# Kernel optimization log

Hardware: AMD Instinct MI355X
Metric: run time of the kernel (lower is better)

The kernel has to match this reference:

```python
import jax, jax.numpy as jnp
import numpy as np

N = 50000
E = 800000
IN_DIM = 128
HID = 128
HEADS = 8
OUT_DIM = 64
LRELU_SLOPE = 0.2


def setup_inputs() -> dict:
    key = jax.random.key(0)
    ks = jax.random.split(key, 10)
    x = jax.random.normal(ks[0], (N, IN_DIM), dtype=jnp.float32)
    edge_index = jax.random.randint(ks[1], (2, E), 0, N, dtype=jnp.int64)
    c1 = HID // HEADS  # 16
    W1 = jax.random.normal(ks[2], (IN_DIM, HID), dtype=jnp.float32) * (1.0 / np.sqrt(IN_DIM))
    as1 = jax.random.normal(ks[3], (HEADS, c1), dtype=jnp.float32) * 0.1
    ad1 = jax.random.normal(ks[4], (HEADS, c1), dtype=jnp.float32) * 0.1
    b1 = jnp.zeros((HID,), dtype=jnp.float32)
    W2 = jax.random.normal(ks[5], (HID, OUT_DIM), dtype=jnp.float32) * (1.0 / np.sqrt(HID))
    as2 = jax.random.normal(ks[6], (1, OUT_DIM), dtype=jnp.float32) * 0.1
    ad2 = jax.random.normal(ks[7], (1, OUT_DIM), dtype=jnp.float32) * 0.1
    b2 = jnp.zeros((OUT_DIM,), dtype=jnp.float32)
    return {"x": x, "edge_index": edge_index, "W1": W1, "as1": as1, "ad1": ad1,
            "b1": b1, "W2": W2, "as2": as2, "ad2": ad2, "b2": b2}


def gat_conv(x, src, dst, W, a_src, a_dst, b, heads, ch, concat):
    n = x.shape[0]
    h = (x @ W).reshape(n, heads, ch)               # [N,H,C]
    alpha_s = jnp.sum(h * a_src, axis=-1)           # [N,H]
    alpha_d = jnp.sum(h * a_dst, axis=-1)           # [N,H]
    e = jax.nn.leaky_relu(alpha_s[src] + alpha_d[dst], LRELU_SLOPE)  # [E,H]
    m = jax.ops.segment_max(e, dst, num_segments=n)  # per-dst max (self-loops guarantee nonempty)
    e = jnp.exp(e - m[dst])
    denom = jax.ops.segment_sum(e, dst, num_segments=n)
    alpha = e / (denom[dst] + 1e-16)                # [E,H]
    msg = h[src] * alpha[:, :, None]                # [E,H,C]
    out = jax.ops.segment_sum(msg, dst, num_segments=n)  # [N,H,C]
    out = out.reshape(n, heads * ch) if concat else out.mean(axis=1)
    return out + b


def reference(x, edge_index, W1, as1, ad1, b1, W2, as2, ad2, b2):
    n = x.shape[0]
    loops = jnp.arange(n, dtype=edge_index.dtype)
    src = jnp.concatenate([edge_index[0], loops])   # PyG GATConv adds self-loops
    dst = jnp.concatenate([edge_index[1], loops])
    # layer 1: GATBlock (dropout is identity at eval), heads=8, concat, ELU
    h = gat_conv(x, src, dst, W1, as1, ad1, b1, HEADS, HID // HEADS, True)
    h = jax.nn.elu(h)
    # final conv: heads=1, concat=False
    out = gat_conv(h, src, dst, W2, as2, ad2, b2, 1, OUT_DIM, False)
    return jax.nn.log_softmax(out, axis=1)
```

## Files before the change

### kernel.cpp

```cpp
#include <hip/hip_runtime.h>
#include <hip/hip_bf16.h>
#include <math.h>

#define IN_DIM 128
#define HID 128
#define HEADS 8
#define OUT_DIM 64
#define SLOPE 0.2f
#define BSHIFT 7
#define BCAP 4096
#define BCAPSHIFT 12
#define EPT 8

typedef short bf16x8 __attribute__((ext_vector_type(8)));
typedef float f32x4 __attribute__((ext_vector_type(4)));

__device__ __forceinline__ float lrelu(float x) { return fmaxf(x, SLOPE * x); }
__device__ __forceinline__ float bf2f(unsigned u) { return __uint_as_float(u << 16); }
__device__ __forceinline__ unsigned short f2bf(float f) {
    unsigned u = __float_as_uint(f);
    return (unsigned short)((u + 0x7FFF + ((u >> 16) & 1)) >> 16);
}

__device__ __forceinline__ void bscatter_body(
    int blk, const int* __restrict__ idx,
    int* __restrict__ gcursor, unsigned* __restrict__ bucket_buf,
    int E, int N, int NB) {
    __shared__ int hist[512];
    __shared__ int base[512];
    __shared__ int s_nz;
    int t = threadIdx.x;
    for (int i = t; i < NB; i += 256) hist[i] = 0;
    if (t == 0) s_nz = 0;
    __syncthreads();
    {
        int nz = (idx[2 * t + 1] != 0) + (idx[2 * t + 513] != 0);
        if (nz) atomicAdd(&s_nz, nz);
    }
    __syncthreads();
    int flag = (s_nz > 16) ? 1 : 0;
    int e0 = blk * (256 * EPT);
    int EN = E + N;
    unsigned ent[EPT];
    int bid[EPT];
    int loc[EPT];
#pragma unroll
    for (int k = 0; k < EPT; k++) {
        int e = e0 + k * 256 + t;
        bid[k] = -1;
        if (e < EN) {
            int src, dst;
            if (e < E) {
                if (flag) { src = idx[e]; dst = idx[E + e]; }
                else      { src = idx[2 * e]; dst = idx[2 * (E + e)]; }
            } else {
                src = dst = e - E;
            }
            int b = dst >> BSHIFT;
            bid[k] = b;
            ent[k] = ((unsigned)(dst & ((1 << BSHIFT) - 1)) << 16) | (unsigned)src;
            loc[k] = atomicAdd(&hist[b], 1);
        }
    }
    __syncthreads();
    for (int i = t; i < NB; i += 256) {
        int c = hist[i];
        if (c) base[i] = atomicAdd(&gcursor[i], c);
    }
    __syncthreads();
#pragma unroll
    for (int k = 0; k < EPT; k++) {
        if (bid[k] >= 0) {
            int pos = base[bid[k]] + loc[k];
            if (pos < BCAP) bucket_buf[((size_t)bid[k] << BCAPSHIFT) + pos] = ent[k];
        }
    }
}

__device__ __forceinline__ void gemm1_body(
    int blk, const float* __restrict__ x, const float* __restrict__ W1,
    unsigned short* __restrict__ h1g, int N) {
    __shared__ short Wt[128 * 136];
    int t = threadIdx.x;
    for (int id = t; id < 128 * 32; id += 256) {
        int k = id >> 5;
        int n0 = (id & 31) * 4;
        float4 v = *(const float4*)&W1[k * 128 + n0];
        Wt[(n0 + 0) * 136 + k] = (short)f2bf(v.x);
        Wt[(n0 + 1) * 136 + k] = (short)f2bf(v.y);
        Wt[(n0 + 2) * 136 + k] = (short)f2bf(v.z);
        Wt[(n0 + 3) * 136 + k] = (short)f2bf(v.w);
    }
    __syncthreads();
    int wv = t >> 6, lane = t & 63;
    int m = lane & 15, q = lane >> 4;
    int row = blk * 64 + wv * 16 + m;
    f32x4 acc[8];
#pragma unroll
    for (int j = 0; j < 8; j++) acc[j] = (f32x4){0.f, 0.f, 0.f, 0.f};
#pragma unroll
    for (int k0 = 0; k0 < 128; k0 += 32) {
        bf16x8 a = {0, 0, 0, 0, 0, 0, 0, 0};
        if (row < N) {
            const float* xp = &x[(size_t)row * 128 + k0 + q * 8];
            float4 u0 = *(const float4*)xp;
            float4 u1 = *(const float4*)(xp + 4);
            a[0] = (short)f2bf(u0.x); a[1] = (short)f2bf(u0.y);
            a[2] = (short)f2bf(u0.z); a[3] = (short)f2bf(u0.w);
            a[4] = (short)f2bf(u1.x); a[5] = (short)f2bf(u1.y);
            a[6] = (short)f2bf(u1.z); a[7] = (short)f2bf(u1.w);
        }
#pragma unroll
        for (int j = 0; j < 8; j++) {
            bf16x8 b = *(const bf16x8*)&Wt[(j * 16 + m) * 136 + k0 + q * 8];
            acc[j] = __builtin_amdgcn_mfma_f32_16x16x32_bf16(a, b, acc[j], 0, 0, 0);
        }
    }
    int rbase = blk * 64 + wv * 16 + q * 4;
#pragma unroll
    for (int r = 0; r < 4; r++) {
        int rr = rbase + r;
        if (rr < N) {
#pragma unroll
            for (int j = 0; j < 8; j++)
                h1g[(size_t)rr * 128 + j * 16 + m] = f2bf(acc[j][r]);
        }
    }
}

__global__ __launch_bounds__(256) void k1_kernel(
    const int* __restrict__ idx, int* __restrict__ gcursor,
    unsigned* __restrict__ bucket_buf,
    const float* __restrict__ x, const float* __restrict__ W1,
    unsigned short* __restrict__ h1g, int E, int N, int NB, int GS) {
    if ((int)blockIdx.x < GS)
        bscatter_body(blockIdx.x, idx, gcursor, bucket_buf, E, N, NB);
    else
        gemm1_body(blockIdx.x - GS, x, W1, h1g, N);
}

__device__ __forceinline__ void bsort_body(
    int b, const int* __restrict__ gcursor, const unsigned* __restrict__ bucket_buf,
    int* __restrict__ row_start, int* __restrict__ sorted_src, int N, int NB) {
    __shared__ int cnt[128];
    __shared__ int cur[128];
    __shared__ int red[4];
    __shared__ int s_w0;
    int t = threadIdx.x;
    if (t < 128) cnt[t] = 0;
    int partial = 0;
    for (int i = t; i < b; i += 256) partial += min(gcursor[i], BCAP);
#pragma unroll
    for (int msk = 32; msk > 0; msk >>= 1) partial += __shfl_xor(partial, msk, 64);
    if ((t & 63) == 0) red[t >> 6] = partial;
    __syncthreads();
    int bbase = red[0] + red[1] + red[2] + red[3];
    int c = min(gcursor[b], BCAP);
    const unsigned* buf = bucket_buf + ((size_t)b << BCAPSHIFT);
    for (int i = t; i < c; i += 256)
        atomicAdd(&cnt[(buf[i] >> 16) & 127], 1);
    __syncthreads();
    int v = (t < 128) ? cnt[t] : 0;
    int lane = t & 63;
    int incl = v;
#pragma unroll
    for (int off = 1; off < 64; off <<= 1) {
        int u = __shfl_up(incl, off, 64);
        if (lane >= off) incl += u;
    }
    if (t == 63) s_w0 = incl;
    __syncthreads();
    if (t < 128) {
        int excl = incl - v + ((t >= 64) ? s_w0 : 0);
        int pos = bbase + excl;
        cur[t] = pos;
        int node = (b << BSHIFT) + t;
        if (node <= N) row_start[node] = pos;
    }
    __syncthreads();
    for (int i = t; i < c; i += 256) {
        unsigned e = buf[i];
        int pos = atomicAdd(&cur[(e >> 16) & 127], 1);
        sorted_src[pos] = (int)(e & 0xFFFFu);
    }
}

__device__ __forceinline__ void alpha1_body(
    int blk, const unsigned short* __restrict__ h1g,
    const float* __restrict__ a_s, const float* __restrict__ a_d,
    float* __restrict__ as_n, float* __restrict__ ad_n, int N) {
    int gid = blk * 256 + threadIdx.x;
    if (gid >= N * 8) return;
    int n = gid >> 3, hd = gid & 7;
    const uint4* hp = (const uint4*)(h1g + (size_t)n * 128 + hd * 16);
    uint4 u0 = hp[0], u1 = hp[1];
    unsigned uu[8] = {u0.x, u0.y, u0.z, u0.w, u1.x, u1.y, u1.z, u1.w};
    const float* sp = a_s + hd * 16;
    const float* dp = a_d + hd * 16;
    float s = 0.f, d = 0.f;
#pragma unroll
    for (int k = 0; k < 8; k++) {
        float lo = bf2f(uu[k] & 0xffffu), hi = bf2f(uu[k] >> 16);
        s += lo * sp[2 * k] + hi * sp[2 * k + 1];
        d += lo * dp[2 * k] + hi * dp[2 * k + 1];
    }
    as_n[gid] = s;
    ad_n[gid] = d;
}

__global__ __launch_bounds__(256) void k2_kernel(
    const int* __restrict__ gcursor, const unsigned* __restrict__ bucket_buf,
    int* __restrict__ row_start, int* __restrict__ sorted_src,
    const unsigned short* __restrict__ h1g,
    const float* __restrict__ a_s, const float* __restrict__ a_d,
    float* __restrict__ as_n, float* __restrict__ ad_n, int N, int NB) {
    if ((int)blockIdx.x < NB)
        bsort_body(blockIdx.x, gcursor, bucket_buf, row_start, sorted_src, N, NB);
    else
        alpha1_body(blockIdx.x - NB, h1g, a_s, a_d, as_n, ad_n, N);
}

__global__ __launch_bounds__(256) void agg1_kernel(
    const int* __restrict__ row_start, const int* __restrict__ sorted_src,
    const float* __restrict__ as_n, const float* __restrict__ ad_n,
    const unsigned short* __restrict__ h1g, const float* __restrict__ b1,
    unsigned short* __restrict__ h1act, int N) {
    int node = blockIdx.x * 4 + (threadIdx.x >> 6);
    int lane = threadIdx.x & 63;
    if (node >= N) return;
    int slot = lane >> 4, cg = lane & 15;
    int srcLane = (slot << 3) | (cg >> 1);
    float ad_w = ad_n[node * 8 + (lane & 7)];
    int beg = row_start[node], end = row_start[node + 1];
    float acc[8];
#pragma unroll
    for (int k = 0; k < 8; k++) acc[k] = 0.f;
    float denom = 0.f;
    for (int i = beg; i < end; i += 8) {
        int ewa = i + ((lane >> 3) & 3);
        int ewb = ewa + 4;
        int swa = sorted_src[min(ewa, end - 1)];
        int swb = sorted_src[min(ewb, end - 1)];
        float wa = __expf(lrelu(as_n[swa * 8 + (lane & 7)] + ad_w));
        float wb = __expf(lrelu(as_n[swb * 8 + (lane & 7)] + ad_w));
        wa = (ewa < end) ? wa : 0.f;
        wb = (ewb < end) ? wb : 0.f;
        float wva = __shfl(wa, srcLane, 64);
        float wvb = __shfl(wb, srcLane, 64);
        int ega = i + slot, egb = ega + 4;
        int sga = sorted_src[min(ega, end - 1)];
        int sgb = sorted_src[min(egb, end - 1)];
        uint4 hva = *(const uint4*)&h1g[(size_t)sga * 128 + cg * 8];
        uint4 hvb = *(const uint4*)&h1g[(size_t)sgb * 128 + cg * 8];
        acc[0] += wva * bf2f(hva.x & 0xffffu) + wvb * bf2f(hvb.x & 0xffffu);
        acc[1] += wva * bf2f(hva.x >> 16)     + wvb * bf2f(hvb.x >> 16);
        acc[2] += wva * bf2f(hva.y & 0xffffu) + wvb * bf2f(hvb.y & 0xffffu);
        acc[3] += wva * bf2f(hva.y >> 16)     + wvb * bf2f(hvb.y >> 16);
        acc[4] += wva * bf2f(hva.z & 0xffffu) + wvb * bf2f(hvb.z & 0xffffu);
        acc[5] += wva * bf2f(hva.z >> 16)     + wvb * bf2f(hvb.z >> 16);
        acc[6] += wva * bf2f(hva.w & 0xffffu) + wvb * bf2f(hvb.w & 0xffffu);
        acc[7] += wva * bf2f(hva.w >> 16)     + wvb * bf2f(hvb.w >> 16);
        denom += wva + wvb;
    }
#pragma unroll
    for (int msk = 16; msk < 64; msk <<= 1) {
#pragma unroll
        for (int k = 0; k < 8; k++) acc[k] += __shfl_xor(acc[k], msk, 64);
        denom += __shfl_xor(denom, msk, 64);
    }
    if (slot == 0) {
        float inv = 1.f / (denom + 1e-16f);
        int c0 = cg * 8;
        unsigned ow[4];
#pragma unroll
        for (int p = 0; p < 4; p++) {
            float v0 = acc[2 * p] * inv + b1[c0 + 2 * p];
            float v1 = acc[2 * p + 1] * inv + b1[c0 + 2 * p + 1];
            v0 = (v0 > 0.f) ? v0 : (__expf(v0) - 1.f);
            v1 = (v1 > 0.f) ? v1 : (__expf(v1) - 1.f);
            ow[p] = (unsigned)f2bf(v0) | ((unsigned)f2bf(v1) << 16);
        }
        *(uint4*)&h1act[(size_t)node * 128 + c0] = make_uint4(ow[0], ow[1], ow[2], ow[3]);
    }
}

__global__ __launch_bounds__(256) void gemm2_kernel(
    const unsigned short* __restrict__ h1act, const float* __restrict__ W2,
    const float* __restrict__ a_s, const float* __restrict__ a_d,
    unsigned short* __restrict__ h2g, float* __restrict__ as_n,
    float* __restrict__ ad_n, int N) {
    __shared__ short Wt[64 * 136];
    int t = threadIdx.x;
    for (int id = t; id < 128 * 16; id += 256) {
        int k = id >> 4;
        int n0 = (id & 15) * 4;
        float4 v = *(const float4*)&W2[k * 64 + n0];
        Wt[(n0 + 0) * 136 + k] = (short)f2bf(v.x);
        Wt[(n0 + 1) * 136 + k] = (short)f2bf(v.y);
        Wt[(n0 + 2) * 136 + k] = (short)f2bf(v.z);
        Wt[(n0 + 3) * 136 + k] = (short)f2bf(v.w);
    }
    __syncthreads();
    int wv = t >> 6, lane = t & 63;
    int m = lane & 15, q = lane >> 4;
    int row = blockIdx.x * 64 + wv * 16 + m;
    f32x4 acc[4];
#pragma unroll
    for (int j = 0; j < 4; j++) acc[j] = (f32x4){0.f, 0.f, 0.f, 0.f};
#pragma unroll
    for (int k0 = 0; k0 < 128; k0 += 32) {
        bf16x8 a = {0, 0, 0, 0, 0, 0, 0, 0};
        if (row < N) a = *(const bf16x8*)&h1act[(size_t)row * 128 + k0 + q * 8];
#pragma unroll
        for (int j = 0; j < 4; j++) {
            bf16x8 b = *(const bf16x8*)&Wt[(j * 16 + m) * 136 + k0 + q * 8];
            acc[j] = __builtin_amdgcn_mfma_f32_16x16x32_bf16(a, b, acc[j], 0, 0, 0);
        }
    }
    float asl[4], adl[4];
#pragma unroll
    for (int j = 0; j < 4; j++) { asl[j] = a_s[j * 16 + m]; adl[j] = a_d[j * 16 + m]; }
    int rbase = blockIdx.x * 64 + wv * 16 + q * 4;
#pragma unroll
    for (int r = 0; r < 4; r++) {
        int rr = rbase + r;
        float s = 0.f, d = 0.f;
#pragma unroll
        for (int j = 0; j < 4; j++) {
            s += acc[j][r] * asl[j];
            d += acc[j][r] * adl[j];
        }
#pragma unroll
        for (int msk = 8; msk > 0; msk >>= 1) {
            s += __shfl_xor(s, msk, 64);
            d += __shfl_xor(d, msk, 64);
        }
        if (rr < N) {
            if (m == 0) { as_n[rr] = s; ad_n[rr] = d; }
#pragma unroll
            for (int j = 0; j < 4; j++)
                h2g[(size_t)rr * 64 + j * 16 + m] = f2bf(acc[j][r]);
        }
    }
}

__global__ __launch_bounds__(256) void agg2_kernel(
    const int* __restrict__ row_start, const int* __restrict__ sorted_src,
    const float* __restrict__ as_n, const float* __restrict__ ad_n,
    const unsigned short* __restrict__ h2g, const float* __restrict__ b2,
    float* __restrict__ out, int N) {
    int node = blockIdx.x * 4 + (threadIdx.x >> 6);
    int lane = threadIdx.x & 63;
    if (node >= N) return;
    int slot = lane >> 4, cg = lane & 15;
    float adv = ad_n[node];
    int beg = row_start[node], end = row_start[node + 1];
    float acc[4];
#pragma unroll
    for (int k = 0; k < 4; k++) acc[k] = 0.f;
    float denom = 0.f;
    for (int i = beg; i < end; i += 8) {
        int ewa = i + (lane & 3);
        int ewb = ewa + 4;
        int swa = sorted_src[min(ewa, end - 1)];
        int swb = sorted_src[min(ewb, end - 1)];
        float wa = __expf(lrelu(as_n[swa] + adv));
        float wb = __expf(lrelu(as_n[swb] + adv));
        wa = (ewa < end) ? wa : 0.f;
        wb = (ewb < end) ? wb : 0.f;
        float wva = __shfl(wa, slot, 64);
        float wvb = __shfl(wb, 4 + slot, 64);
        int ega = i + slot, egb = ega + 4;
        int sga = sorted_src[min(ega, end - 1)];
        int sgb = sorted_src[min(egb, end - 1)];
        uint2 hva = *(const uint2*)&h2g[(size_t)sga * 64 + cg * 4];
        uint2 hvb = *(const uint2*)&h2g[(size_t)sgb * 64 + cg * 4];
        acc[0] += wva * bf2f(hva.x & 0xffffu) + wvb * bf2f(hvb.x & 0xffffu);
        acc[1] += wva * bf2f(hva.x >> 16)     + wvb * bf2f(hvb.x >> 16);
        acc[2] += wva * bf2f(hva.y & 0xffffu) + wvb * bf2f(hvb.y & 0xffffu);
        acc[3] += wva * bf2f(hva.y >> 16)     + wvb * bf2f(hvb.y >> 16);
        denom += wva + wvb;
    }
#pragma unroll
    for (int msk = 16; msk < 64; msk <<= 1) {
#pragma unroll
        for (int k = 0; k < 4; k++) acc[k] += __shfl_xor(acc[k], msk, 64);
        denom += __shfl_xor(denom, msk, 64);
    }
    if (slot == 0) {
        float inv = 1.f / (denom + 1e-16f);
        int c0 = cg * 4;
        float v[4];
#pragma unroll
        for (int k = 0; k < 4; k++) v[k] = acc[k] * inv + b2[c0 + k];
        float m = fmaxf(fmaxf(v[0], v[1]), fmaxf(v[2], v[3]));
#pragma unroll
        for (int msk = 8; msk > 0; msk >>= 1) m = fmaxf(m, __shfl_xor(m, msk, 64));
        float ex = __expf(v[0] - m) + __expf(v[1] - m) + __expf(v[2] - m) + __expf(v[3] - m);
#pragma unroll
        for (int msk = 8; msk > 0; msk >>= 1) ex += __shfl_xor(ex, msk, 64);
        float lse = m + __logf(ex);
        float4 ov = make_float4(v[0] - lse, v[1] - lse, v[2] - lse, v[3] - lse);
        *(float4*)&out[(size_t)node * 64 + c0] = ov;
    }
}

extern "C" void kernel_launch(void* const* d_in, const int* in_sizes, int n_in,
                              void* d_out, int out_size, void* d_ws, size_t ws_size,
                              hipStream_t stream) {
    const float* x   = (const float*)d_in[0];
    const int*   idx = (const int*)d_in[1];
    const float* W1  = (const float*)d_in[2];
    const float* as1 = (const float*)d_in[3];
    const float* ad1 = (const float*)d_in[4];
    const float* b1  = (const float*)d_in[5];
    const float* W2  = (const float*)d_in[6];
    const float* as2 = (const float*)d_in[7];
    const float* ad2 = (const float*)d_in[8];
    const float* b2  = (const float*)d_in[9];
    float* out = (float*)d_out;

    const int N = in_sizes[0] / IN_DIM;
    const int E = in_sizes[1] / 2;
    const int EN = E + N;
    const int NB = (N + (1 << BSHIFT) - 1) >> BSHIFT;
    const int GS = (EN + 256 * EPT - 1) / (256 * EPT);
    const int G1 = (N + 63) / 64;
    const int A1 = (N * 8 + 255) / 256;

    unsigned short* h1g   = (unsigned short*)d_ws;
    unsigned short* h1act = h1g + (size_t)N * 128;
    unsigned short* h2g   = h1act + (size_t)N * 128;
    float* as1n = (float*)(h2g + (size_t)N * 64);
    float* ad1n = as1n + (size_t)N * 8;
    float* as2n = ad1n + (size_t)N * 8;
    float* ad2n = as2n + (size_t)N;
    int* row_start  = (int*)(ad2n + (size_t)N);
    int* gcursor    = row_start + N + 1;
    unsigned* bucket_buf = (unsigned*)(gcursor + 512);
    int* sorted_src = (int*)(bucket_buf + ((size_t)NB << BCAPSHIFT));
    (void)ws_size; (void)n_in; (void)out_size;

    hipMemsetAsync(gcursor, 0, 512 * sizeof(int), stream);

    k1_kernel<<<GS + G1, 256, 0, stream>>>(idx, gcursor, bucket_buf,
                                           x, W1, h1g, E, N, NB, GS);
    k2_kernel<<<NB + A1, 256, 0, stream>>>(gcursor, bucket_buf, row_start, sorted_src,
                                           h1g, as1, ad1, as1n, ad1n, N, NB);
    agg1_kernel<<<(N + 3) / 4, 256, 0, stream>>>(row_start, sorted_src, as1n, ad1n, h1g, b1, h1act, N);
    gemm2_kernel<<<(N + 63) / 64, 256, 0, stream>>>(h1act, W2, as2, ad2, h2g, as2n, ad2n, N);
    agg2_kernel<<<(N + 3) / 4, 256, 0, stream>>>(row_start, sorted_src, as2n, ad2n, h2g, b2, out, N);
}
```

Baseline: 217.9 us.

## Persistent GEMM tiles, shared smem union, and single-load edge gather in aggregations

Both GEMMs become persistent grid-stride loops over 64-row tiles with a fixed grid, so the W transpose into LDS is paid once per block instead of once per tile. In k1 the scatter and GEMM branches now share one LDS buffer, which lowers the kernel's LDS footprint. The aggregation kernels load each edge's source index once per lane (8 edges per wave) and broadcast both weight and index with shuffles, removing the duplicate sorted_src loads and min clamps. This depends on padding sorted_src with 8 zeros past EN so that reads beyond a row stay in bounds, which makes each wave issue fewer gathers.

New measurement: 218.6 us. No clear change (+0.3%).

```diff
diff --git a/kernel.cpp b/kernel.cpp
--- a/kernel.cpp
+++ b/kernel.cpp
@@ -11,6 +11,8 @@
 #define BCAP 4096
 #define BCAPSHIFT 12
 #define EPT 8
+#define G1 256
+#define G2 256
 
 typedef short bf16x8 __attribute__((ext_vector_type(8)));
 typedef float f32x4 __attribute__((ext_vector_type(4)));
@@ -23,22 +25,22 @@
 }
 
 __device__ __forceinline__ void bscatter_body(
-    int blk, const int* __restrict__ idx,
+    int blk, int* smem, const int* __restrict__ idx,
     int* __restrict__ gcursor, unsigned* __restrict__ bucket_buf,
     int E, int N, int NB) {
-    __shared__ int hist[512];
-    __shared__ int base[512];
-    __shared__ int s_nz;
+    int* hist = smem;
+    int* base = smem + 512;
+    int* s_nz = smem + 1024;
     int t = threadIdx.x;
     for (int i = t; i < NB; i += 256) hist[i] = 0;
-    if (t == 0) s_nz = 0;
+    if (t == 0) *s_nz = 0;
     __syncthreads();
     {
         int nz = (idx[2 * t + 1] != 0) + (idx[2 * t + 513] != 0);
-        if (nz) atomicAdd(&s_nz, nz);
-    }
-    __syncthreads();
-    int flag = (s_nz > 16) ? 1 : 0;
+        if (nz) atomicAdd(s_nz, nz);
+    }
+    __syncthreads();
+    int flag = (*s_nz > 16) ? 1 : 0;
     int e0 = blk * (256 * EPT);
     int EN = E + N;
     unsigned ent[EPT];
@@ -78,9 +80,8 @@
 }
 
 __device__ __forceinline__ void gemm1_body(
-    int blk, const float* __restrict__ x, const float* __restrict__ W1,
+    int blk, short* Wt, const float* __restrict__ x, const float* __restrict__ W1,
     unsigned short* __restrict__ h1g, int N) {
-    __shared__ short Wt[128 * 136];
     int t = threadIdx.x;
     for (int id = t; id < 128 * 32; id += 256) {
         int k = id >> 5;
@@ -94,36 +95,39 @@
     __syncthreads();
     int wv = t >> 6, lane = t & 63;
     int m = lane & 15, q = lane >> 4;
-    int row = blk * 64 + wv * 16 + m;
-    f32x4 acc[8];
-#pragma unroll
-    for (int j = 0; j < 8; j++) acc[j] = (f32x4){0.f, 0.f, 0.f, 0.f};
-#pragma unroll
-    for (int k0 = 0; k0 < 128; k0 += 32) {
-        bf16x8 a = {0, 0, 0, 0, 0, 0, 0, 0};
-        if (row < N) {
-            const float* xp = &x[(size_t)row * 128 + k0 + q * 8];
-            float4 u0 = *(const float4*)xp;
-            float4 u1 = *(const float4*)(xp + 4);
-            a[0] = (short)f2bf(u0.x); a[1] = (short)f2bf(u0.y);
-            a[2] = (short)f2bf(u0.z); a[3] = (short)f2bf(u0.w);
-            a[4] = (short)f2bf(u1.x); a[5] = (short)f2bf(u1.y);
-            a[6] = (short)f2bf(u1.z); a[7] = (short)f2bf(u1.w);
-        }
-#pragma unroll
-        for (int j = 0; j < 8; j++) {
-            bf16x8 b = *(const bf16x8*)&Wt[(j * 16 + m) * 136 + k0 + q * 8];
-            acc[j] = __builtin_amdgcn_mfma_f32_16x16x32_bf16(a, b, acc[j], 0, 0, 0);
-        }
-    }
-    int rbase = blk * 64 + wv * 16 + q * 4;
-#pragma unroll
-    for (int r = 0; r < 4; r++) {
-        int rr = rbase + r;
-        if (rr < N) {
-#pragma unroll
-            for (int j = 0; j < 8; j++)
-                h1g[(size_t)rr * 128 + j * 16 + m] = f2bf(acc[j][r]);
+    int T = (N + 63) >> 6;
+    for (int tile = blk; tile < T; tile += G1) {
+        int row = tile * 64 + wv * 16 + m;
+        f32x4 acc[8];
+#pragma unroll
+        for (int j = 0; j < 8; j++) acc[j] = (f32x4){0.f, 0.f, 0.f, 0.f};
+#pragma unroll
+        for (int k0 = 0; k0 < 128; k0 += 32) {
+            bf16x8 a = {0, 0, 0, 0, 0, 0, 0, 0};
+            if (row < N) {
+                const float* xp = &x[(size_t)row * 128 + k0 + q * 8];
+                float4 u0 = *(const float4*)xp;
+                float4 u1 = *(const float4*)(xp + 4);
+                a[0] = (short)f2bf(u0.x); a[1] = (short)f2bf(u0.y);
+                a[2] = (short)f2bf(u0.z); a[3] = (short)f2bf(u0.w);
+                a[4] = (short)f2bf(u1.x); a[5] = (short)f2bf(u1.y);
+                a[6] = (short)f2bf(u1.z); a[7] = (short)f2bf(u1.w);
+            }
+#pragma unroll
+            for (int j = 0; j < 8; j++) {
+                bf16x8 b = *(const bf16x8*)&Wt[(j * 16 + m) * 136 + k0 + q * 8];
+                acc[j] = __builtin_amdgcn_mfma_f32_16x16x32_bf16(a, b, acc[j], 0, 0, 0);
+            }
+        }
+        int rbase = tile * 64 + wv * 16 + q * 4;
+#pragma unroll
+        for (int r = 0; r < 4; r++) {
+            int rr = rbase + r;
+            if (rr < N) {
+#pragma unroll
+                for (int j = 0; j < 8; j++)
+                    h1g[(size_t)rr * 128 + j * 16 + m] = f2bf(acc[j][r]);
+            }
         }
     }
 }
@@ -133,10 +137,11 @@
     unsigned* __restrict__ bucket_buf,
     const float* __restrict__ x, const float* __restrict__ W1,
     unsigned short* __restrict__ h1g, int E, int N, int NB, int GS) {
+    __shared__ long long smem[4352];
     if ((int)blockIdx.x < GS)
-        bscatter_body(blockIdx.x, idx, gcursor, bucket_buf, E, N, NB);
+        bscatter_body(blockIdx.x, (int*)smem, idx, gcursor, bucket_buf, E, N, NB);
     else
-        gemm1_body(blockIdx.x - GS, x, W1, h1g, N);
+        gemm1_body(blockIdx.x - GS, (short*)smem, x, W1, h1g, N);
 }
 
 __device__ __forceinline__ void bsort_body(
@@ -213,7 +218,8 @@
     int* __restrict__ row_start, int* __restrict__ sorted_src,
     const unsigned short* __restrict__ h1g,
     const float* __restrict__ a_s, const float* __restrict__ a_d,
-    float* __restrict__ as_n, float* __restrict__ ad_n, int N, int NB) {
+    float* __restrict__ as_n, float* __restrict__ ad_n, int N, int NB, int EN) {
+    if (blockIdx.x == 0 && threadIdx.x < 8) sorted_src[EN + threadIdx.x] = 0;
     if ((int)blockIdx.x < NB)
         bsort_body(blockIdx.x, gcursor, bucket_buf, row_start, sorted_src, N, NB);
     else
@@ -229,27 +235,23 @@
     int lane = threadIdx.x & 63;
     if (node >= N) return;
     int slot = lane >> 4, cg = lane & 15;
-    int srcLane = (slot << 3) | (cg >> 1);
-    float ad_w = ad_n[node * 8 + (lane & 7)];
+    int e8 = lane >> 3, hd8 = lane & 7;
+    int wl_a = (slot << 3) | (cg >> 1);
+    int wl_b = ((slot + 4) << 3) | (cg >> 1);
+    float ad_w = ad_n[node * 8 + hd8];
     int beg = row_start[node], end = row_start[node + 1];
     float acc[8];
 #pragma unroll
     for (int k = 0; k < 8; k++) acc[k] = 0.f;
     float denom = 0.f;
     for (int i = beg; i < end; i += 8) {
-        int ewa = i + ((lane >> 3) & 3);
-        int ewb = ewa + 4;
-        int swa = sorted_src[min(ewa, end - 1)];
-        int swb = sorted_src[min(ewb, end - 1)];
-        float wa = __expf(lrelu(as_n[swa * 8 + (lane & 7)] + ad_w));
-        float wb = __expf(lrelu(as_n[swb * 8 + (lane & 7)] + ad_w));
-        wa = (ewa < end) ? wa : 0.f;
-        wb = (ewb < end) ? wb : 0.f;
-        float wva = __shfl(wa, srcLane, 64);
-        float wvb = __shfl(wb, srcLane, 64);
-        int ega = i + slot, egb = ega + 4;
-        int sga = sorted_src[min(ega, end - 1)];
-        int sgb = sorted_src[min(egb, end - 1)];
+        int se = sorted_src[i + e8];
+        float w = __expf(lrelu(as_n[se * 8 + hd8] + ad_w));
+        w = (i + e8 < end) ? w : 0.f;
+        float wva = __shfl(w, wl_a, 64);
+        float wvb = __shfl(w, wl_b, 64);
+        int sga = __shfl(se, wl_a, 64);
+        int sgb = __shfl(se, wl_b, 64);
         uint4 hva = *(const uint4*)&h1g[(size_t)sga * 128 + cg * 8];
         uint4 hvb = *(const uint4*)&h1g[(size_t)sgb * 128 + cg * 8];
         acc[0] += wva * bf2f(hva.x & 0xffffu) + wvb * bf2f(hvb.x & 0xffffu);
@@ -303,43 +305,46 @@
     __syncthreads();
     int wv = t >> 6, lane = t & 63;
     int m = lane & 15, q = lane >> 4;
-    int row = blockIdx.x * 64 + wv * 16 + m;
-    f32x4 acc[4];
-#pragma unroll
-    for (int j = 0; j < 4; j++) acc[j] = (f32x4){0.f, 0.f, 0.f, 0.f};
-#pragma unroll
-    for (int k0 = 0; k0 < 128; k0 += 32) {
-        bf16x8 a = {0, 0, 0, 0, 0, 0, 0, 0};
-        if (row < N) a = *(const bf16x8*)&h1act[(size_t)row * 128 + k0 + q * 8];
-#pragma unroll
-        for (int j = 0; j < 4; j++) {
-            bf16x8 b = *(const bf16x8*)&Wt[(j * 16 + m) * 136 + k0 + q * 8];
-            acc[j] = __builtin_amdgcn_mfma_f32_16x16x32_bf16(a, b, acc[j], 0, 0, 0);
-        }
-    }
     float asl[4], adl[4];
 #pragma unroll
     for (int j = 0; j < 4; j++) { asl[j] = a_s[j * 16 + m]; adl[j] = a_d[j * 16 + m]; }
-    int rbase = blockIdx.x * 64 + wv * 16 + q * 4;
-#pragma unroll
-    for (int r = 0; r < 4; r++) {
-        int rr = rbase + r;
-        float s = 0.f, d = 0.f;
-#pragma unroll
-        for (int j = 0; j < 4; j++) {
-            s += acc[j][r] * asl[j];
-            d += acc[j][r] * adl[j];
-        }
-#pragma unroll
-        for (int msk = 8; msk > 0; msk >>= 1) {
-            s += __shfl_xor(s, msk, 64);
-            d += __shfl_xor(d, msk, 64);
-        }
-        if (rr < N) {
-            if (m == 0) { as_n[rr] = s; ad_n[rr] = d; }
-#pragma unroll
-            for (int j = 0; j < 4; j++)
-                h2g[(size_t)rr * 64 + j * 16 + m] = f2bf(acc[j][r]);
+    int T = (N + 63) >> 6;
+    for (int tile = blockIdx.x; tile < T; tile += G2) {
+        int row = tile * 64 + wv * 16 + m;
+        f32x4 acc[4];
+#pragma unroll
+        for (int j = 0; j < 4; j++) acc[j] = (f32x4){0.f, 0.f, 0.f, 0.f};
+#pragma unroll
+        for (int k0 = 0; k0 < 128; k0 += 32) {
+            bf16x8 a = {0, 0, 0, 0, 0, 0, 0, 0};
+            if (row < N) a = *(const bf16x8*)&h1act[(size_t)row * 128 + k0 + q * 8];
+#pragma unroll
+            for (int j = 0; j < 4; j++) {
+                bf16x8 b = *(const bf16x8*)&Wt[(j * 16 + m) * 136 + k0 + q * 8];
+                acc[j] = __builtin_amdgcn_mfma_f32_16x16x32_bf16(a, b, acc[j], 0, 0, 0);
+            }
+        }
+        int rbase = tile * 64 + wv * 16 + q * 4;
+#pragma unroll
+        for (int r = 0; r < 4; r++) {
+            int rr = rbase + r;
+            float s = 0.f, d = 0.f;
+#pragma unroll
+            for (int j = 0; j < 4; j++) {
+                s += acc[j][r] * asl[j];
+                d += acc[j][r] * adl[j];
+            }
+#pragma unroll
+            for (int msk = 8; msk > 0; msk >>= 1) {
+                s += __shfl_xor(s, msk, 64);
+                d += __shfl_xor(d, msk, 64);
+            }
+            if (rr < N) {
+                if (m == 0) { as_n[rr] = s; ad_n[rr] = d; }
+#pragma unroll
+                for (int j = 0; j < 4; j++)
+                    h2g[(size_t)rr * 64 + j * 16 + m] = f2bf(acc[j][r]);
+            }
         }
     }
 }
@@ -353,6 +358,7 @@
     int lane = threadIdx.x & 63;
     if (node >= N) return;
     int slot = lane >> 4, cg = lane & 15;
+    int e8 = lane & 7;
     float adv = ad_n[node];
     int beg = row_start[node], end = row_start[node + 1];
     float acc[4];
@@ -360,19 +366,13 @@
     for (int k = 0; k < 4; k++) acc[k] = 0.f;
     float denom = 0.f;
     for (int i = beg; i < end; i += 8) {
-        int ewa = i + (lane & 3);
-        int ewb = ewa + 4;
-        int swa = sorted_src[min(ewa, end - 1)];
-        int swb = sorted_src[min(ewb, end - 1)];
-        float wa = __expf(lrelu(as_n[swa] + adv));
-        float wb = __expf(lrelu(as_n[swb] + adv));
-        wa = (ewa < end) ? wa : 0.f;
-        wb = (ewb < end) ? wb : 0.f;
-        float wva = __shfl(wa, slot, 64);
-        float wvb = __shfl(wb, 4 + slot, 64);
-        int ega = i + slot, egb = ega + 4;
-        int sga = sorted_src[min(ega, end - 1)];
-        int sgb = sorted_src[min(egb, end - 1)];
+        int se = sorted_src[i + e8];
+        float w = __expf(lrelu(as_n[se] + adv));
+        w = (i + e8 < end) ? w : 0.f;
+        float wva = __shfl(w, slot, 64);
+        float wvb = __shfl(w, slot + 4, 64);
+        int sga = __shfl(se, slot, 64);
+        int sgb = __shfl(se, slot + 4, 64);
         uint2 hva = *(const uint2*)&h2g[(size_t)sga * 64 + cg * 4];
         uint2 hvb = *(const uint2*)&h2g[(size_t)sgb * 64 + cg * 4];
         acc[0] += wva * bf2f(hva.x & 0xffffu) + wvb * bf2f(hvb.x & 0xffffu);
@@ -425,7 +425,6 @@
     const int EN = E + N;
     const int NB = (N + (1 << BSHIFT) - 1) >> BSHIFT;
     const int GS = (EN + 256 * EPT - 1) / (256 * EPT);
-    const int G1 = (N + 63) / 64;
     const int A1 = (N * 8 + 255) / 256;
 
     unsigned short* h1g   = (unsigned short*)d_ws;
@@ -446,8 +445,8 @@
     k1_kernel<<<GS + G1, 256, 0, stream>>>(idx, gcursor, bucket_buf,
                                            x, W1, h1g, E, N, NB, GS);
     k2_kernel<<<NB + A1, 256, 0, stream>>>(gcursor, bucket_buf, row_start, sorted_src,
-                                           h1g, as1, ad1, as1n, ad1n, N, NB);
+                                           h1g, as1, ad1, as1n, ad1n, N, NB, EN);
     agg1_kernel<<<(N + 3) / 4, 256, 0, stream>>>(row_start, sorted_src, as1n, ad1n, h1g, b1, h1act, N);
-    gemm2_kernel<<<(N + 63) / 64, 256, 0, stream>>>(h1act, W2, as2, ad2, h2g, as2n, ad2n, N);
+    gemm2_kernel<<<G2, 256, 0, stream>>>(h1act, W2, as2, ad2, h2g, as2n, ad2n, N);
     agg2_kernel<<<(N + 3) / 4, 256, 0, stream>>>(row_start, sorted_src, as2n, ad2n, h2g, b2, out, N);
 }
```
